# Kernel optimization log

Measured on AMD Instinct MI355X. Metric: run time of the kernel, lower is better.

Reference implementation:

```python
import jax, jax.numpy as jnp
import numpy as np

B, N, DIM = 4, 4096, 1024
HEADS, DIM_HEAD, BSZ, EPS = 8, 64, 16, 1e-8
INNER = HEADS * DIM_HEAD


def setup_inputs() -> dict:
    key = jax.random.key(0)
    k1, k2, k3 = jax.random.split(key, 3)
    x = jax.random.normal(k1, (B, N, DIM), dtype=jnp.float32)
    # torch nn.Linear weights are [out, in]; scale ~ fan_in^-0.5 for stable exp()
    w_qkv = jax.random.normal(k2, (3 * INNER, DIM), dtype=jnp.float32) * (DIM ** -0.5)
    w_out = jax.random.normal(k3, (DIM, INNER), dtype=jnp.float32) * (INNER ** -0.5)
    b_out = jnp.zeros((DIM,), dtype=jnp.float32)
    return {"x": x, "w_qkv": w_qkv, "w_out": w_out, "b_out": b_out}


def _to_bh(t, b, n):
    # 'b n (h d) -> (b h) n d'
    return t.reshape(b, n, HEADS, DIM_HEAD).transpose(0, 2, 1, 3).reshape(b * HEADS, n, DIM_HEAD)


def _to_blocks(t):
    # 'b (n z) d -> b n z d'
    return t.reshape(t.shape[0], -1, BSZ, DIM_HEAD)


def _calc_Y_and_A(qb, kb, vb):
    S = jnp.einsum('bnid,bnjd->bnij', qb, kb)   # block-local scores
    A = jnp.exp(S)
    y = jnp.einsum('bnij,bnjd->bnid', A, vb)
    return y.reshape(y.shape[0], -1, DIM_HEAD), A.sum(-1).reshape(A.shape[0], -1)


def _hattention(x, w_qkv, w_out, b_out):
    b, n, _ = x.shape
    qkv = x @ w_qkv.T
    q, k, v = jnp.split(qkv, 3, axis=-1)
    q, k, v = (_to_bh(t, b, n) for t in (q, k, v))
    q = q * (DIM_HEAD ** -0.5)

    num_levels = int(np.log2(n // BSZ)) - 1
    qkvs = [(q, k, v)]
    for _ in range(num_levels):
        q = q.reshape(q.shape[0], -1, 2, DIM_HEAD).mean(axis=2)
        k = k.reshape(k.shape[0], -1, 2, DIM_HEAD).mean(axis=2)
        v = v.reshape(v.shape[0], -1, 2, DIM_HEAD).sum(axis=2)
        qkvs.append((q, k, v))
    top_level = qkvs[0]
    coarse_levels = qkvs[1:][::-1]  # coarsest first

    Ys = []
    for (ql, kl, vl) in coarse_levels:
        qb, kb, vb = map(_to_blocks, (ql, kl, vl))
        bh, nb = kb.shape[0], kb.shape[1]
        # flip sibling key blocks: 'b (n r) z d' with r=2 reversed
        kb = kb.reshape(bh, nb // 2, 2, BSZ, DIM_HEAD)[:, :, ::-1].reshape(bh, nb, BSZ, DIM_HEAD)
        Ys.append(_calc_Y_and_A(qb, kb, vb))
    Ys.append(_calc_Y_and_A(*map(_to_blocks, top_level)))

    Y, A = Ys[0]
    for y_l, a_l in Ys[1:]:
        Y = jnp.repeat(Y, 2, axis=1) + y_l
        A = jnp.repeat(A, 2, axis=1) + a_l

    out = Y / (A + EPS)[..., None]
    # '(b h) n d -> b n (h d)'
    out = out.reshape(b, HEADS, n, DIM_HEAD).transpose(0, 2, 1, 3).reshape(b, n, INNER)
    return out @ w_out.T + b_out


def reference(x, w_qkv, w_out, b_out):
    return _hattention(x, w_qkv, w_out, b_out)
```

## Files before the change

### kernel.cpp

```cpp
#include <hip/hip_runtime.h>
#include <hip/hip_bf16.h>


typedef __bf16 bf16x8 __attribute__((ext_vector_type(8)));
typedef float floatx4 __attribute__((ext_vector_type(4)));
typedef unsigned short ushortx8 __attribute__((ext_vector_type(8)));
typedef unsigned int uintx4 __attribute__((ext_vector_type(4)));

#define ROWS_PER_BH 8160

__device__ __forceinline__ void g2lds16(const void* g, void* l) {
  __builtin_amdgcn_global_load_lds(
      (const __attribute__((address_space(1))) void*)g,
      (__attribute__((address_space(3))) void*)l, 16, 0, 0);
}

__device__ __forceinline__ unsigned short f2bu(float x) {
  __hip_bfloat16 h = __float2bfloat16(x);
  return *(unsigned short*)&h;
}
__device__ __forceinline__ float bu2f(unsigned short u) {
  __hip_bfloat16 h = *(__hip_bfloat16*)&u;
  return __bfloat162float(h);
}

__global__ __launch_bounds__(256) void f2b3_kernel(const float* __restrict__ x,
                                                   const float* __restrict__ wq,
                                                   const float* __restrict__ wo,
                                                   __hip_bfloat16* __restrict__ xb,
                                                   __hip_bfloat16* __restrict__ wqb,
                                                   __hip_bfloat16* __restrict__ wob) {
  int i0 = (blockIdx.x * 256 + threadIdx.x) * 4;
  const float* s;
  __hip_bfloat16* d;
  if (i0 < 16777216) {
    s = x; d = xb;
  } else if (i0 < 16777216 + 1572864) {
    s = wq + (i0 - 16777216); d = wqb + (i0 - 16777216);
    float4 v = *(const float4*)s;
    d[0] = __float2bfloat16(v.x); d[1] = __float2bfloat16(v.y);
    d[2] = __float2bfloat16(v.z); d[3] = __float2bfloat16(v.w);
    return;
  } else {
    s = wo + (i0 - 16777216 - 1572864); d = wob + (i0 - 16777216 - 1572864);
    float4 v = *(const float4*)s;
    d[0] = __float2bfloat16(v.x); d[1] = __float2bfloat16(v.y);
    d[2] = __float2bfloat16(v.z); d[3] = __float2bfloat16(v.w);
    return;
  }
  float4 v = *(const float4*)(s + i0);
  d[i0 + 0] = __float2bfloat16(v.x);
  d[i0 + 1] = __float2bfloat16(v.y);
  d[i0 + 2] = __float2bfloat16(v.z);
  d[i0 + 3] = __float2bfloat16(v.w);
}

template <int K>
__device__ __forceinline__ void gemm_core(const unsigned short* __restrict__ A,
                                          const unsigned short* __restrict__ B,
                                          unsigned short* ldsA, unsigned short* ldsB,
                                          int tM, int tN, floatx4 acc[4][4]) {
  const int tid = threadIdx.x;
  const int lane = tid & 63, w = tid >> 6;
  const int wm = w >> 1, wn = w & 1;
  const int lr = lane >> 3;
  const int gch = (lane & 7) ^ lr;
  const unsigned short* Ag = A + (size_t)(tM + w * 32 + lr) * K + gch * 8;
  const unsigned short* Bg = B + (size_t)(tN + w * 32 + lr) * K + gch * 8;
  unsigned short* lA = &ldsA[w * 2048 + lane * 8];
  unsigned short* lB = &ldsB[w * 2048 + lane * 8];

  const int rA = wm * 64 + (lane & 15);
  const int rB = wn * 64 + (lane & 15);
  const int quad = lane >> 4;
  const int sw = lane & 7;

  for (int kt = 0; kt < K; kt += 64) {
    __syncthreads();
#pragma unroll
    for (int c = 0; c < 4; c++) {
      g2lds16(Ag + (size_t)(c * 8) * K + kt, lA + c * 512);
      g2lds16(Bg + (size_t)(c * 8) * K + kt, lB + c * 512);
    }
    __syncthreads();
#pragma unroll
    for (int kk = 0; kk < 2; kk++) {
      bf16x8 af[4], bv[4];
#pragma unroll
      for (int i = 0; i < 4; i++)
        af[i] = *(const bf16x8*)&ldsA[(rA + i * 16) * 64 + (((kk * 4 + quad) ^ sw) * 8)];
#pragma unroll
      for (int j = 0; j < 4; j++)
        bv[j] = *(const bf16x8*)&ldsB[(rB + j * 16) * 64 + (((kk * 4 + quad) ^ sw) * 8)];
#pragma unroll
      for (int i = 0; i < 4; i++)
#pragma unroll
        for (int j = 0; j < 4; j++)
          acc[i][j] = __builtin_amdgcn_mfma_f32_16x16x32_bf16(af[i], bv[j], acc[i][j], 0, 0, 0);
    }
  }
}

__global__ __launch_bounds__(256) void gemm_qkv_kernel(
    const unsigned short* __restrict__ A,
    const unsigned short* __restrict__ B,
    __hip_bfloat16* __restrict__ qp, __hip_bfloat16* __restrict__ kp,
    __hip_bfloat16* __restrict__ vp) {
  __shared__ unsigned short ldsA[128 * 64];
  __shared__ unsigned short ldsB[128 * 64];
  const int lane = threadIdx.x & 63, w = threadIdx.x >> 6;
  const int wm = w >> 1, wn = w & 1;
  const int tM = blockIdx.x * 128, tN = blockIdx.y * 128;

  floatx4 acc[4][4];
#pragma unroll
  for (int i = 0; i < 4; i++)
#pragma unroll
    for (int j = 0; j < 4; j++) acc[i][j] = (floatx4){0.f, 0.f, 0.f, 0.f};

  gemm_core<1024>(A, B, ldsA, ldsB, tM, tN, acc);

  const int quad = lane >> 4, m15 = lane & 15;
#pragma unroll
  for (int i = 0; i < 4; i++) {
#pragma unroll
    for (int j = 0; j < 4; j++) {
      const int c = tN + wn * 64 + j * 16 + m15;
      const int tensor = c >> 9;
      const int rem = c & 511;
      const int h = rem >> 6, d = rem & 63;
      __hip_bfloat16* dstbuf = (tensor == 0) ? qp : ((tensor == 1) ? kp : vp);
      const float scale = (tensor == 0) ? 0.125f : 1.0f;
#pragma unroll
      for (int r = 0; r < 4; r++) {
        const int m = tM + wm * 64 + i * 16 + quad * 4 + r;
        const int b = m >> 12, n = m & 4095;
        size_t dst = ((size_t)(b * 8 + h) * ROWS_PER_BH + n) * 64 + d;
        dstbuf[dst] = __float2bfloat16(acc[i][j][r] * scale);
      }
      float s4 = acc[i][j][0] + acc[i][j][1] + acc[i][j][2] + acc[i][j][3];
      s4 += __shfl_xor(s4, 16, 64);
      s4 += __shfl_xor(s4, 32, 64);
      if (quad == 0) {
        const int mrow = tM + wm * 64 + i * 16;
        const int b = mrow >> 12, n4 = (mrow & 4095) >> 4;
        const float val = (tensor == 0) ? s4 * (0.125f / 16.f)
                         : ((tensor == 1) ? s4 * (1.f / 16.f) : s4);
        dstbuf[((size_t)(b * 8 + h) * ROWS_PER_BH + 7680 + n4) * 64 + d] =
            __float2bfloat16(val);
      }
    }
  }
}

__global__ __launch_bounds__(256) void gemm_out_kernel(
    const unsigned short* __restrict__ A,
    const unsigned short* __restrict__ B,
    const float* __restrict__ bias, float* __restrict__ out) {
  __shared__ unsigned short ldsA[128 * 64];
  __shared__ unsigned short ldsB[128 * 64];
  const int lane = threadIdx.x & 63, w = threadIdx.x >> 6;
  const int wm = w >> 1, wn = w & 1;
  const int tM = blockIdx.x * 128, tN = blockIdx.y * 128;

  floatx4 acc[4][4];
#pragma unroll
  for (int i = 0; i < 4; i++)
#pragma unroll
    for (int j = 0; j < 4; j++) acc[i][j] = (floatx4){0.f, 0.f, 0.f, 0.f};

  gemm_core<512>(A, B, ldsA, ldsB, tM, tN, acc);

  const int quad = lane >> 4;
#pragma unroll
  for (int i = 0; i < 4; i++) {
#pragma unroll
    for (int j = 0; j < 4; j++) {
      const int c = tN + wn * 64 + j * 16 + (lane & 15);
      const float bb = bias[c];
#pragma unroll
      for (int r = 0; r < 4; r++) {
        const int m = tM + wm * 64 + i * 16 + quad * 4 + r;
        out[(size_t)m * 1024 + c] = acc[i][j][r] + bb;
      }
    }
  }
}

__global__ __launch_bounds__(512, 1) void coarse47_kernel(
    const unsigned short* __restrict__ qp, const unsigned short* __restrict__ kp,
    const unsigned short* __restrict__ vp, __hip_bfloat16* __restrict__ yall,
    float* __restrict__ aall) {
  __shared__ __align__(16) unsigned short qs[256 * 64];
  __shared__ __align__(16) unsigned short ks[256 * 64];
  __shared__ __align__(16) unsigned short vs[256 * 64];
  __shared__ __align__(16) unsigned short vT[8][64 * 24];

  const int tid = threadIdx.x;
  const int w = tid >> 6, lane = tid & 63;
  const int m = lane & 15, q = lane >> 4;
  const int bh = blockIdx.x;
  const size_t base = (size_t)bh * ROWS_PER_BH;
  const size_t g0 = (base + 7680) * 64;

  auto sidx = [](int r, int d) {
    return r * 64 + (((d >> 3) ^ (r & 7)) << 3) + (d & 7);
  };
  unsigned short* vtw = vT[w];

  {
    const int srow = tid >> 3;
    const int sch = (tid & 7) ^ (srow & 7);
    const size_t gofs = (size_t)srow * 64 + sch * 8;
#pragma unroll
    for (int it = 0; it < 4; it++) {
      const size_t gi = g0 + (size_t)it * 4096 + gofs;
      g2lds16(qp + gi, &qs[it * 4096 + tid * 8]);
      g2lds16(kp + gi, &ks[it * 4096 + tid * 8]);
      g2lds16(vp + gi, &vs[it * 4096 + tid * 8]);
    }
  }
  __syncthreads();

  auto attn_block = [&](int level, int blk, bool flip, floatx4 yout[4]) -> float {
    const int kb = flip ? (blk ^ 1) : blk;
    const int Rq = (blk * 16 + m) << level;
    const int Rk = (kb * 16 + m) << level;
    const bf16x8 ka0 = *(const bf16x8*)&ks[sidx(Rk, q * 8)];
    const bf16x8 ka1 = *(const bf16x8*)&ks[sidx(Rk, 32 + q * 8)];
    const bf16x8 qb0 = *(const bf16x8*)&qs[sidx(Rq, q * 8)];
    const bf16x8 qb1 = *(const bf16x8*)&qs[sidx(Rq, 32 + q * 8)];
    const ushortx8 v0 = *(const ushortx8*)&vs[sidx(Rq, q * 16)];
    const ushortx8 v1 = *(const ushortx8*)&vs[sidx(Rq, q * 16 + 8)];
#pragma unroll
    for (int j = 0; j < 8; j++) vtw[(q * 16 + j) * 24 + m] = v0[j];
#pragma unroll
    for (int j = 0; j < 8; j++) vtw[(q * 16 + 8 + j) * 24 + m] = v1[j];

    floatx4 s = (floatx4){0.f, 0.f, 0.f, 0.f};
    s = __builtin_amdgcn_mfma_f32_16x16x32_bf16(ka0, qb0, s, 0, 0, 0);
    s = __builtin_amdgcn_mfma_f32_16x16x32_bf16(ka1, qb1, s, 0, 0, 0);

    unsigned short pb0 = f2bu(__expf(s[0])), pb1 = f2bu(__expf(s[1]));
    unsigned short pb2 = f2bu(__expf(s[2])), pb3 = f2bu(__expf(s[3]));
    float asum = bu2f(pb0) + bu2f(pb1) + bu2f(pb2) + bu2f(pb3);
    asum += __shfl_xor(asum, 16, 64);
    asum += __shfl_xor(asum, 32, 64);

    unsigned int d0 = (unsigned int)pb0 | ((unsigned int)pb1 << 16);
    unsigned int d1 = (unsigned int)pb2 | ((unsigned int)pb3 << 16);
    const int s0l = m + 32 * (q & 1);
    unsigned int u0 = __shfl(d0, s0l, 64);
    unsigned int u1 = __shfl(d1, s0l, 64);
    unsigned int u2 = __shfl(d0, s0l + 16, 64);
    unsigned int u3 = __shfl(d1, s0l + 16, 64);
    union { uintx4 i; bf16x8 b; } pau;
    pau.i = (q < 2) ? (uintx4){u0, u1, u2, u3} : (uintx4){0u, 0u, 0u, 0u};
    const bf16x8 pa = pau.b;

#pragma unroll
    for (int cc = 0; cc < 4; cc++) {
      union { uintx4 i; bf16x8 b; } bvu;
      bvu.i = (uintx4){0u, 0u, 0u, 0u};
      if (q < 2) bvu.b = *(const bf16x8*)&vtw[(cc * 16 + m) * 24 + q * 8];
      floatx4 y = (floatx4){0.f, 0.f, 0.f, 0.f};
      y = __builtin_amdgcn_mfma_f32_16x16x32_bf16(pa, bvu.b, y, 0, 0, 0);
      yout[cc] = y;
    }
    return asum;
  };

  auto pyr = [&](int l) {
    const int nOut = 256 >> l;
    for (int e = tid; e < nOut * 32; e += 512) {
      const int i = e >> 5, dp = (e & 31) * 2;
      const int ra = i << l, rb = ra + (1 << (l - 1));
      const int ia = sidx(ra, dp), ib = sidx(rb, dp);
      unsigned short q0 = f2bu(0.5f * (bu2f(qs[ia]) + bu2f(qs[ib])));
      unsigned short q1 = f2bu(0.5f * (bu2f(qs[ia + 1]) + bu2f(qs[ib + 1])));
      unsigned short k0 = f2bu(0.5f * (bu2f(ks[ia]) + bu2f(ks[ib])));
      unsigned short k1 = f2bu(0.5f * (bu2f(ks[ia + 1]) + bu2f(ks[ib + 1])));
      unsigned short v0 = f2bu(bu2f(vs[ia]) + bu2f(vs[ib]));
      unsigned short v1 = f2bu(bu2f(vs[ia + 1]) + bu2f(vs[ib + 1]));
      qs[ia] = q0; qs[ia + 1] = q1;
      ks[ia] = k0; ks[ia + 1] = k1;
      vs[ia] = v0; vs[ia + 1] = v1;
    }
  };

  auto emit = [&](int ro, int blk, const floatx4 yt[4], float a) {
    const size_t arow = base + ro + blk * 16;
    if (q == 0) aall[arow + m] = a;
#pragma unroll
    for (int cc = 0; cc < 4; cc++)
#pragma unroll
      for (int r = 0; r < 4; r++)
        yall[(arow + q * 4 + r) * 64 + cc * 16 + m] = __float2bfloat16(yt[cc][r]);
  };

  {
    floatx4 yt[4];
#pragma unroll
    for (int t = 0; t < 2; t++) {
      const int blk = w + t * 8;
      float a = attn_block(0, blk, true, yt);
      emit(7680, blk, yt, a);
    }
  }
  __syncthreads();
  pyr(1);
  __syncthreads();
  {
    floatx4 yt[4];
    float a = attn_block(1, w, true, yt);
    emit(7936, w, yt, a);
  }
  __syncthreads();
  pyr(2);
  __syncthreads();
  if (w < 4) {
    floatx4 yt[4];
    float a = attn_block(2, w, true, yt);
    emit(8064, w, yt, a);
  }
  __syncthreads();
  pyr(3);
  __syncthreads();
  if (w < 2) {
    floatx4 yt[4];
    float a = attn_block(3, w, true, yt);
    emit(8128, w, yt, a);
  }
}

__global__ __launch_bounds__(512, 1) void fused03_kernel(
    const unsigned short* __restrict__ qp, const unsigned short* __restrict__ kp,
    const unsigned short* __restrict__ vp, const unsigned short* __restrict__ yall,
    const float* __restrict__ aall, __hip_bfloat16* __restrict__ Ub) {
  __shared__ __align__(16) unsigned short qs[256 * 64];
  __shared__ __align__(16) unsigned short ks[256 * 64];
  __shared__ __align__(16) unsigned short vs[256 * 64];
  __shared__ unsigned short ylds[224 * 72];
  __shared__ float alds[480];
  __shared__ __align__(16) unsigned short vT[8][64 * 24];

  const int tid = threadIdx.x;
  const int w = tid >> 6, lane = tid & 63;
  const int m = lane & 15, q = lane >> 4;
  const int c = blockIdx.x, bh = blockIdx.y;
  const size_t base = (size_t)bh * ROWS_PER_BH;
  const size_t g0 = (base + c * 256) * 64;

  auto sidx = [](int r, int d) {
    return r * 64 + (((d >> 3) ^ (r & 7)) << 3) + (d & 7);
  };
  unsigned short* vtw = vT[w];

  {
    const int srow = tid >> 3;
    const int sch = (tid & 7) ^ (srow & 7);
    const size_t gofs = (size_t)srow * 64 + sch * 8;
#pragma unroll
    for (int it = 0; it < 4; it++) {
      const size_t gi = g0 + (size_t)it * 4096 + gofs;
      g2lds16(qp + gi, &qs[it * 4096 + tid * 8]);
      g2lds16(kp + gi, &ks[it * 4096 + tid * 8]);
      g2lds16(vp + gi, &vs[it * 4096 + tid * 8]);
    }
  }
  __syncthreads();

  auto attn_block = [&](int level, int blk, bool flip, floatx4 yout[4]) -> float {
    const int kb = flip ? (blk ^ 1) : blk;
    const int Rq = (blk * 16 + m) << level;
    const int Rk = (kb * 16 + m) << level;
    const bf16x8 ka0 = *(const bf16x8*)&ks[sidx(Rk, q * 8)];
    const bf16x8 ka1 = *(const bf16x8*)&ks[sidx(Rk, 32 + q * 8)];
    const bf16x8 qb0 = *(const bf16x8*)&qs[sidx(Rq, q * 8)];
    const bf16x8 qb1 = *(const bf16x8*)&qs[sidx(Rq, 32 + q * 8)];
    const ushortx8 v0 = *(const ushortx8*)&vs[sidx(Rq, q * 16)];
    const ushortx8 v1 = *(const ushortx8*)&vs[sidx(Rq, q * 16 + 8)];
#pragma unroll
    for (int j = 0; j < 8; j++) vtw[(q * 16 + j) * 24 + m] = v0[j];
#pragma unroll
    for (int j = 0; j < 8; j++) vtw[(q * 16 + 8 + j) * 24 + m] = v1[j];

    floatx4 s = (floatx4){0.f, 0.f, 0.f, 0.f};
    s = __builtin_amdgcn_mfma_f32_16x16x32_bf16(ka0, qb0, s, 0, 0, 0);
    s = __builtin_amdgcn_mfma_f32_16x16x32_bf16(ka1, qb1, s, 0, 0, 0);

    unsigned short pb0 = f2bu(__expf(s[0])), pb1 = f2bu(__expf(s[1]));
    unsigned short pb2 = f2bu(__expf(s[2])), pb3 = f2bu(__expf(s[3]));
    float asum = bu2f(pb0) + bu2f(pb1) + bu2f(pb2) + bu2f(pb3);
    asum += __shfl_xor(asum, 16, 64);
    asum += __shfl_xor(asum, 32, 64);

    unsigned int d0 = (unsigned int)pb0 | ((unsigned int)pb1 << 16);
    unsigned int d1 = (unsigned int)pb2 | ((unsigned int)pb3 << 16);
    const int s0l = m + 32 * (q & 1);
    unsigned int u0 = __shfl(d0, s0l, 64);
    unsigned int u1 = __shfl(d1, s0l, 64);
    unsigned int u2 = __shfl(d0, s0l + 16, 64);
    unsigned int u3 = __shfl(d1, s0l + 16, 64);
    union { uintx4 i; bf16x8 b; } pau;
    pau.i = (q < 2) ? (uintx4){u0, u1, u2, u3} : (uintx4){0u, 0u, 0u, 0u};
    const bf16x8 pa = pau.b;

#pragma unroll
    for (int cc = 0; cc < 4; cc++) {
      union { uintx4 i; bf16x8 b; } bvu;
      bvu.i = (uintx4){0u, 0u, 0u, 0u};
      if (q < 2) bvu.b = *(const bf16x8*)&vtw[(cc * 16 + m) * 24 + q * 8];
      floatx4 y = (floatx4){0.f, 0.f, 0.f, 0.f};
      y = __builtin_amdgcn_mfma_f32_16x16x32_bf16(pa, bvu.b, y, 0, 0, 0);
      yout[cc] = y;
    }
    return asum;
  };

  auto pyr = [&](int l) {
    const int nOut = 256 >> l;
    for (int e = tid; e < nOut * 32; e += 512) {
      const int i = e >> 5, dp = (e & 31) * 2;
      const int ra = i << l, rb = ra + (1 << (l - 1));
      const int ia = sidx(ra, dp), ib = sidx(rb, dp);
      unsigned short q0 = f2bu(0.5f * (bu2f(qs[ia]) + bu2f(qs[ib])));
      unsigned short q1 = f2bu(0.5f * (bu2f(qs[ia + 1]) + bu2f(qs[ib + 1])));
      unsigned short k0 = f2bu(0.5f * (bu2f(ks[ia]) + bu2f(ks[ib])));
      unsigned short k1 = f2bu(0.5f * (bu2f(ks[ia + 1]) + bu2f(ks[ib + 1])));
      unsigned short v0 = f2bu(bu2f(vs[ia]) + bu2f(vs[ib]));
      unsigned short v1 = f2bu(bu2f(vs[ia + 1]) + bu2f(vs[ib + 1]));
      qs[ia] = q0; qs[ia + 1] = q1;
      ks[ia] = k0; ks[ia + 1] = k1;
      vs[ia] = v0; vs[ia + 1] = v1;
    }
  };

  floatx4 y0reg[2][4];
#pragma unroll
  for (int t = 0; t < 2; t++) {
    const int blk = w + t * 8;
    float a0 = attn_block(0, blk, false, y0reg[t]);
    if (q == 0) alds[224 + blk * 16 + m] = a0;
  }
  __syncthreads();

  pyr(1);
  __syncthreads();
  {
    floatx4 yt[4];
    const int blk = w;
    float a = attn_block(1, blk, true, yt);
    if (q == 0) alds[blk * 16 + m] = a;
#pragma unroll
    for (int cc = 0; cc < 4; cc++)
#pragma unroll
      for (int r = 0; r < 4; r++)
        ylds[(blk * 16 + q * 4 + r) * 72 + cc * 16 + m] = f2bu(yt[cc][r]);
  }
  __syncthreads();
  pyr(2);
  __syncthreads();
  if (w < 4) {
    floatx4 yt[4];
    const int blk = w;
    float a = attn_block(2, blk, true, yt);
    if (q == 0) alds[128 + blk * 16 + m] = a;
#pragma unroll
    for (int cc = 0; cc < 4; cc++)
#pragma unroll
      for (int r = 0; r < 4; r++)
        ylds[(128 + blk * 16 + q * 4 + r) * 72 + cc * 16 + m] = f2bu(yt[cc][r]);
  }
  __syncthreads();
  pyr(3);
  __syncthreads();
  if (w < 2) {
    floatx4 yt[4];
    const int blk = w;
    float a = attn_block(3, blk, true, yt);
    if (q == 0) alds[192 + blk * 16 + m] = a;
#pragma unroll
    for (int cc = 0; cc < 4; cc++)
#pragma unroll
      for (int r = 0; r < 4; r++)
        ylds[(192 + blk * 16 + q * 4 + r) * 72 + cc * 16 + m] = f2bu(yt[cc][r]);
  }
  __syncthreads();

  const int bO = bh >> 3, hO = bh & 7;
#pragma unroll
  for (int t = 0; t < 2; t++) {
    const int blk = w + t * 8;
    const int i4 = c * 16 + blk;
    const size_t r4 = base + 7680 + i4;
    const size_t r5 = base + 7936 + (i4 >> 1);
    const size_t r6 = base + 8064 + (i4 >> 2);
    const size_t r7 = base + 8128 + (i4 >> 3);
    const float acoarse = aall[r4] + aall[r5] + aall[r6] + aall[r7];

    float inv[4];
#pragma unroll
    for (int r = 0; r < 4; r++) {
      const int row = blk * 16 + q * 4 + r;
      const float atot = alds[224 + row] + alds[row >> 1] +
                         alds[128 + (row >> 2)] + alds[192 + (row >> 3)] +
                         acoarse + 1e-8f;
      inv[r] = 1.0f / atot;
    }

#pragma unroll
    for (int cc = 0; cc < 4; cc++) {
      const int col = cc * 16 + m;
      const float yc = bu2f(yall[r4 * 64 + col]) + bu2f(yall[r5 * 64 + col]) +
                       bu2f(yall[r6 * 64 + col]) + bu2f(yall[r7 * 64 + col]);
#pragma unroll
      for (int r = 0; r < 4; r++) {
        const int row = blk * 16 + q * 4 + r;
        const float num = y0reg[t][cc][r] + bu2f(ylds[(row >> 1) * 72 + col]) +
                          bu2f(ylds[(128 + (row >> 2)) * 72 + col]) +
                          bu2f(ylds[(192 + (row >> 3)) * 72 + col]) + yc;
        Ub[((size_t)bO * 4096 + c * 256 + row) * 512 + hO * 64 + col] =
            __float2bfloat16(num * inv[r]);
      }
    }
  }
}

extern "C" void kernel_launch(void* const* d_in, const int* in_sizes, int n_in,
                              void* d_out, int out_size, void* d_ws, size_t ws_size,
                              hipStream_t stream) {
  const float* x     = (const float*)d_in[0];
  const float* w_qkv = (const float*)d_in[1];
  const float* w_out = (const float*)d_in[2];
  const float* b_out = (const float*)d_in[3];
  float* out = (float*)d_out;

  char* ws = (char*)d_ws;
  __hip_bfloat16* xb    = (__hip_bfloat16*)(ws + 0);
  __hip_bfloat16* wqkvb = (__hip_bfloat16*)(ws + 33554432);
  __hip_bfloat16* wob   = (__hip_bfloat16*)(ws + 36700160);
  __hip_bfloat16* qp    = (__hip_bfloat16*)(ws + 37748736);
  __hip_bfloat16* kp    = (__hip_bfloat16*)(ws + 71172096);
  __hip_bfloat16* vp    = (__hip_bfloat16*)(ws + 104595456);
  __hip_bfloat16* yall  = (__hip_bfloat16*)(ws + 138018816);
  float* aall           = (float*)(ws + 171442176);
  __hip_bfloat16* Ub    = (__hip_bfloat16*)(ws + 172486656);

  f2b3_kernel<<<18432, 256, 0, stream>>>(x, w_qkv, w_out, xb, wqkvb, wob);

  gemm_qkv_kernel<<<dim3(128, 12), 256, 0, stream>>>(
      (const unsigned short*)xb, (const unsigned short*)wqkvb, qp, kp, vp);

  coarse47_kernel<<<32, 512, 0, stream>>>(
      (const unsigned short*)qp, (const unsigned short*)kp,
      (const unsigned short*)vp, yall, aall);

  fused03_kernel<<<dim3(16, 32), 512, 0, stream>>>(
      (const unsigned short*)qp, (const unsigned short*)kp,
      (const unsigned short*)vp, (const unsigned short*)yall, aall, Ub);

  gemm_out_kernel<<<dim3(128, 8), 256, 0, stream>>>(
      (const unsigned short*)Ub, (const unsigned short*)wob, b_out, out);
}
```

Baseline: 247.1 us.

## Vectorize bf16 conversion, change LDS swizzles, split QKV GEMM into two launches

The fp32-to-bf16 conversion kernel now handles 8 elements per thread with a single 16-byte store instead of four scalar stores, halving the grid. The LDS swizzle for q/k/v tiles now mixes bits r>>3 into the XOR, and the per-wave V-transpose buffer gets a per-column-group skew, both aimed at reducing bank conflicts. The QKV GEMM is split into two half-M launches via a row offset argument, which adds a launch without an obvious benefit.

```diff
diff --git a/kernel.cpp b/kernel.cpp
--- a/kernel.cpp
+++ b/kernel.cpp
@@ -30,29 +30,22 @@
                                                    __hip_bfloat16* __restrict__ xb,
                                                    __hip_bfloat16* __restrict__ wqb,
                                                    __hip_bfloat16* __restrict__ wob) {
-  int i0 = (blockIdx.x * 256 + threadIdx.x) * 4;
+  int i0 = (blockIdx.x * 256 + threadIdx.x) * 8;
   const float* s;
   __hip_bfloat16* d;
   if (i0 < 16777216) {
-    s = x; d = xb;
+    s = x + i0; d = xb + i0;
   } else if (i0 < 16777216 + 1572864) {
     s = wq + (i0 - 16777216); d = wqb + (i0 - 16777216);
-    float4 v = *(const float4*)s;
-    d[0] = __float2bfloat16(v.x); d[1] = __float2bfloat16(v.y);
-    d[2] = __float2bfloat16(v.z); d[3] = __float2bfloat16(v.w);
-    return;
   } else {
     s = wo + (i0 - 16777216 - 1572864); d = wob + (i0 - 16777216 - 1572864);
-    float4 v = *(const float4*)s;
-    d[0] = __float2bfloat16(v.x); d[1] = __float2bfloat16(v.y);
-    d[2] = __float2bfloat16(v.z); d[3] = __float2bfloat16(v.w);
-    return;
-  }
-  float4 v = *(const float4*)(s + i0);
-  d[i0 + 0] = __float2bfloat16(v.x);
-  d[i0 + 1] = __float2bfloat16(v.y);
-  d[i0 + 2] = __float2bfloat16(v.z);
-  d[i0 + 3] = __float2bfloat16(v.w);
+  }
+  float4 v0 = *(const float4*)s;
+  float4 v1 = *(const float4*)(s + 4);
+  ushortx8 o;
+  o[0] = f2bu(v0.x); o[1] = f2bu(v0.y); o[2] = f2bu(v0.z); o[3] = f2bu(v0.w);
+  o[4] = f2bu(v1.x); o[5] = f2bu(v1.y); o[6] = f2bu(v1.z); o[7] = f2bu(v1.w);
+  *(ushortx8*)d = o;
 }
 
 template <int K>
@@ -105,12 +98,12 @@
     const unsigned short* __restrict__ A,
     const unsigned short* __restrict__ B,
     __hip_bfloat16* __restrict__ qp, __hip_bfloat16* __restrict__ kp,
-    __hip_bfloat16* __restrict__ vp) {
+    __hip_bfloat16* __restrict__ vp, int tMoff) {
   __shared__ unsigned short ldsA[128 * 64];
   __shared__ unsigned short ldsB[128 * 64];
   const int lane = threadIdx.x & 63, w = threadIdx.x >> 6;
   const int wm = w >> 1, wn = w & 1;
-  const int tM = blockIdx.x * 128, tN = blockIdx.y * 128;
+  const int tM = tMoff + blockIdx.x * 128, tN = blockIdx.y * 128;
 
   floatx4 acc[4][4];
 #pragma unroll
@@ -187,6 +180,12 @@
   }
 }
 
+__device__ __forceinline__ int swzf(int r) { return (r ^ (r >> 3)) & 7; }
+__device__ __forceinline__ int sidx(int r, int d) {
+  return r * 64 + (((d >> 3) ^ swzf(r)) << 3) + (d & 7);
+}
+#define VT_SZ 1600
+
 __global__ __launch_bounds__(512, 1) void coarse47_kernel(
     const unsigned short* __restrict__ qp, const unsigned short* __restrict__ kp,
     const unsigned short* __restrict__ vp, __hip_bfloat16* __restrict__ yall,
@@ -194,7 +193,7 @@
   __shared__ __align__(16) unsigned short qs[256 * 64];
   __shared__ __align__(16) unsigned short ks[256 * 64];
   __shared__ __align__(16) unsigned short vs[256 * 64];
-  __shared__ __align__(16) unsigned short vT[8][64 * 24];
+  __shared__ __align__(16) unsigned short vT[8][VT_SZ];
 
   const int tid = threadIdx.x;
   const int w = tid >> 6, lane = tid & 63;
@@ -203,14 +202,11 @@
   const size_t base = (size_t)bh * ROWS_PER_BH;
   const size_t g0 = (base + 7680) * 64;
 
-  auto sidx = [](int r, int d) {
-    return r * 64 + (((d >> 3) ^ (r & 7)) << 3) + (d & 7);
-  };
   unsigned short* vtw = vT[w];
 
   {
     const int srow = tid >> 3;
-    const int sch = (tid & 7) ^ (srow & 7);
+    const int sch = (tid & 7) ^ swzf(srow);
     const size_t gofs = (size_t)srow * 64 + sch * 8;
 #pragma unroll
     for (int it = 0; it < 4; it++) {
@@ -233,9 +229,9 @@
     const ushortx8 v0 = *(const ushortx8*)&vs[sidx(Rq, q * 16)];
     const ushortx8 v1 = *(const ushortx8*)&vs[sidx(Rq, q * 16 + 8)];
 #pragma unroll
-    for (int j = 0; j < 8; j++) vtw[(q * 16 + j) * 24 + m] = v0[j];
-#pragma unroll
-    for (int j = 0; j < 8; j++) vtw[(q * 16 + 8 + j) * 24 + m] = v1[j];
+    for (int j = 0; j < 8; j++) vtw[q * 16 + (q * 16 + j) * 24 + m] = v0[j];
+#pragma unroll
+    for (int j = 0; j < 8; j++) vtw[q * 16 + (q * 16 + 8 + j) * 24 + m] = v1[j];
 
     floatx4 s = (floatx4){0.f, 0.f, 0.f, 0.f};
     s = __builtin_amdgcn_mfma_f32_16x16x32_bf16(ka0, qb0, s, 0, 0, 0);
@@ -262,7 +258,7 @@
     for (int cc = 0; cc < 4; cc++) {
       union { uintx4 i; bf16x8 b; } bvu;
       bvu.i = (uintx4){0u, 0u, 0u, 0u};
-      if (q < 2) bvu.b = *(const bf16x8*)&vtw[(cc * 16 + m) * 24 + q * 8];
+      if (q < 2) bvu.b = *(const bf16x8*)&vtw[cc * 16 + (cc * 16 + m) * 24 + q * 8];
       floatx4 y = (floatx4){0.f, 0.f, 0.f, 0.f};
       y = __builtin_amdgcn_mfma_f32_16x16x32_bf16(pa, bvu.b, y, 0, 0, 0);
       yout[cc] = y;
@@ -342,7 +338,7 @@
   __shared__ __align__(16) unsigned short vs[256 * 64];
   __shared__ unsigned short ylds[224 * 72];
   __shared__ float alds[480];
-  __shared__ __align__(16) unsigned short vT[8][64 * 24];
+  __shared__ __align__(16) unsigned short vT[8][VT_SZ];
 
   const int tid = threadIdx.x;
   const int w = tid >> 6, lane = tid & 63;
@@ -351,14 +347,11 @@
   const size_t base = (size_t)bh * ROWS_PER_BH;
   const size_t g0 = (base + c * 256) * 64;
 
-  auto sidx = [](int r, int d) {
-    return r * 64 + (((d >> 3) ^ (r & 7)) << 3) + (d & 7);
-  };
   unsigned short* vtw = vT[w];
 
   {
     const int srow = tid >> 3;
-    const int sch = (tid & 7) ^ (srow & 7);
+    const int sch = (tid & 7) ^ swzf(srow);
     const size_t gofs = (size_t)srow * 64 + sch * 8;
 #pragma unroll
     for (int it = 0; it < 4; it++) {
@@ -381,9 +374,9 @@
     const ushortx8 v0 = *(const ushortx8*)&vs[sidx(Rq, q * 16)];
     const ushortx8 v1 = *(const ushortx8*)&vs[sidx(Rq, q * 16 + 8)];
 #pragma unroll
-    for (int j = 0; j < 8; j++) vtw[(q * 16 + j) * 24 + m] = v0[j];
-#pragma unroll
-    for (int j = 0; j < 8; j++) vtw[(q * 16 + 8 + j) * 24 + m] = v1[j];
+    for (int j = 0; j < 8; j++) vtw[q * 16 + (q * 16 + j) * 24 + m] = v0[j];
+#pragma unroll
+    for (int j = 0; j < 8; j++) vtw[q * 16 + (q * 16 + 8 + j) * 24 + m] = v1[j];
 
     floatx4 s = (floatx4){0.f, 0.f, 0.f, 0.f};
     s = __builtin_amdgcn_mfma_f32_16x16x32_bf16(ka0, qb0, s, 0, 0, 0);
@@ -410,7 +403,7 @@
     for (int cc = 0; cc < 4; cc++) {
       union { uintx4 i; bf16x8 b; } bvu;
       bvu.i = (uintx4){0u, 0u, 0u, 0u};
-      if (q < 2) bvu.b = *(const bf16x8*)&vtw[(cc * 16 + m) * 24 + q * 8];
+      if (q < 2) bvu.b = *(const bf16x8*)&vtw[cc * 16 + (cc * 16 + m) * 24 + q * 8];
       floatx4 y = (floatx4){0.f, 0.f, 0.f, 0.f};
       y = __builtin_amdgcn_mfma_f32_16x16x32_bf16(pa, bvu.b, y, 0, 0, 0);
       yout[cc] = y;
@@ -547,10 +540,12 @@
   float* aall           = (float*)(ws + 171442176);
   __hip_bfloat16* Ub    = (__hip_bfloat16*)(ws + 172486656);
 
-  f2b3_kernel<<<18432, 256, 0, stream>>>(x, w_qkv, w_out, xb, wqkvb, wob);
-
-  gemm_qkv_kernel<<<dim3(128, 12), 256, 0, stream>>>(
-      (const unsigned short*)xb, (const unsigned short*)wqkvb, qp, kp, vp);
+  f2b3_kernel<<<9216, 256, 0, stream>>>(x, w_qkv, w_out, xb, wqkvb, wob);
+
+  gemm_qkv_kernel<<<dim3(64, 12), 256, 0, stream>>>(
+      (const unsigned short*)xb, (const unsigned short*)wqkvb, qp, kp, vp, 0);
+  gemm_qkv_kernel<<<dim3(64, 12), 256, 0, stream>>>(
+      (const unsigned short*)xb, (const unsigned short*)wqkvb, qp, kp, vp, 8192);
 
   coarse47_kernel<<<32, 512, 0, stream>>>(
       (const unsigned short*)qp, (const unsigned short*)kp,
```

Result: slower. 271.1 us (+9.7%).
